# Kernel optimization log

Measured on AMD Instinct MI355X. Metric: run time of the kernel, lower is better.

Reference implementation:

```python
import jax, jax.numpy as jnp
import numpy as np

B, S, P, D, H, L, DF, O = 8, 1024, 128, 256, 4, 4, 1024, 10
DH = D // H  # 64
EPS = 1e-5


def get_positional_embeddings(seq_len, d):
    i = np.arange(seq_len, dtype=np.float64)[:, None]
    j = np.arange(d, dtype=np.float64)[None, :]
    even = np.sin(i / 10000 ** (j / d))
    odd = np.cos(i / 10000 ** ((j - 1) / d))
    return jnp.asarray(np.where(j % 2 == 0, even, odd), dtype=jnp.float32)


def layernorm(x, g, b):
    m = jnp.mean(x, axis=-1, keepdims=True)
    v = jnp.mean(jnp.square(x - m), axis=-1, keepdims=True)
    return (x - m) * jax.lax.rsqrt(v + EPS) * g + b


def setup_inputs() -> dict:
    key = jax.random.key(0)
    ks = jax.random.split(key, 20)
    w = lambda k, shp: (jax.random.normal(k, shp, dtype=jnp.float32) * 0.02)
    return {
        "images": jax.random.normal(ks[0], (B, S, P), dtype=jnp.float32),
        "Wp": w(ks[1], (D, P)), "bp": jnp.zeros((D,), jnp.float32),
        "cls": jax.random.uniform(ks[2], (1, D), dtype=jnp.float32),
        "pos": get_positional_embeddings(S + 1, D),
        "ln1_g": jnp.ones((L, D), jnp.float32), "ln1_b": jnp.zeros((L, D), jnp.float32),
        "Wq": w(ks[3], (L, H, DH, DH)), "bq": jnp.zeros((L, H, DH), jnp.float32),
        "Wk": w(ks[4], (L, H, DH, DH)), "bk": jnp.zeros((L, H, DH), jnp.float32),
        "Wv": w(ks[5], (L, H, DH, DH)), "bv": jnp.zeros((L, H, DH), jnp.float32),
        "ln2_g": jnp.ones((L, D), jnp.float32), "ln2_b": jnp.zeros((L, D), jnp.float32),
        "W1": w(ks[6], (L, DF, D)), "b1": jnp.zeros((L, DF), jnp.float32),
        "W2": w(ks[7], (L, D, DF)), "b2": jnp.zeros((L, D), jnp.float32),
        "Wo": w(ks[8], (O, D)), "bo": jnp.zeros((O,), jnp.float32),
    }


def msa(x, Wq, bq, Wk, bk, Wv, bv):
    b, s, _ = x.shape
    xh = x.reshape(b, s, H, DH)  # split heads along feature dim
    # torch Linear: y = x @ W.T + b, per head
    q = jnp.einsum("bshd,hed->bhse", xh, Wq) + bq[None, :, None, :]
    k = jnp.einsum("bshd,hed->bhse", xh, Wk) + bk[None, :, None, :]
    v = jnp.einsum("bshd,hed->bhse", xh, Wv) + bv[None, :, None, :]
    scores = jnp.einsum("bhqd,bhkd->bhqk", q, k) / (DH ** 0.5)
    attn = jax.nn.softmax(scores, axis=-1)
    out = jnp.einsum("bhqk,bhkd->bhqd", attn, v)  # [b,h,s,dh]
    return out.transpose(0, 2, 1, 3).reshape(b, s, D)  # hstack heads


def reference(images, Wp, bp, cls, pos, ln1_g, ln1_b, Wq, bq, Wk, bk, Wv, bv,
              ln2_g, ln2_b, W1, b1, W2, b2, Wo, bo):
    tokens = jnp.einsum("bsp,dp->bsd", images, Wp) + bp
    x = jnp.concatenate([jnp.broadcast_to(cls[None], (B, 1, D)), tokens], axis=1)
    x = x + pos[None]
    for l in range(L):
        x = x + msa(layernorm(x, ln1_g[l], ln1_b[l]), Wq[l], bq[l], Wk[l], bk[l], Wv[l], bv[l])
        h = layernorm(x, ln2_g[l], ln2_b[l])
        h = jax.nn.gelu(jnp.einsum("bsd,fd->bsf", h, W1[l]) + b1[l], approximate=False)
        x = x + jnp.einsum("bsf,df->bsd", h, W2[l]) + b2[l]
    logits = x[:, 0] @ Wo.T + bo
    return jax.nn.softmax(logits, axis=-1)
```

## Files before the change

kernel.cpp:

```cpp
#include <hip/hip_runtime.h>
#include <hip/hip_bf16.h>
#include <cmath>

constexpr int B  = 8;
constexpr int S  = 1024;
constexpr int P  = 128;
constexpr int D  = 256;
constexpr int H  = 4;
constexpr int L  = 4;
constexpr int DF = 1024;
constexpr int O  = 10;
constexpr int DH = D / H;
constexpr int SP = S + 1;
constexpr int N  = B * SP;
constexpr int KVPAD = 1088;

typedef short bf16x8 __attribute__((ext_vector_type(8)));
typedef float f32x4 __attribute__((ext_vector_type(4)));
typedef float f32x16 __attribute__((ext_vector_type(16)));
typedef unsigned int u32;
typedef unsigned short u16;

static __device__ __forceinline__ u16 f2b(float f) {
    __hip_bfloat16 h = __float2bfloat16(f);
    u16 u; __builtin_memcpy(&u, &h, 2);
    return u;
}
static __device__ __forceinline__ float b2f(u16 u) {
    u32 uu = (u32)u << 16; float f; __builtin_memcpy(&f, &uu, 4);
    return f;
}
static __device__ __forceinline__ u32 pk2(float a, float b) {
    return (u32)f2b(a) | ((u32)f2b(b) << 16);
}
static __device__ __forceinline__ void gload_lds16(const void* g, void* l) {
    __builtin_amdgcn_global_load_lds((const __attribute__((address_space(1))) unsigned int*)g,
                                     (__attribute__((address_space(3))) unsigned int*)l, 16, 0, 0);
}

__global__ void cvt_all(const float* __restrict__ s0, u16* __restrict__ d0, int n0,
                        const float* __restrict__ s1, u16* __restrict__ d1, int n1,
                        const float* __restrict__ s2, u16* __restrict__ d2, int n2,
                        const float* __restrict__ s3, u16* __restrict__ d3, int n3) {
    int y = blockIdx.y;
    const float* s = y == 0 ? s0 : y == 1 ? s1 : y == 2 ? s2 : s3;
    u16* d = y == 0 ? d0 : y == 1 ? d1 : y == 2 ? d2 : d3;
    int n = y == 0 ? n0 : y == 1 ? n1 : y == 2 ? n2 : n3;
    int i = blockIdx.x * 256 + threadIdx.x;
    if (i < n) {
        float4 v = ((const float4*)s)[i];
        ushort4 o;
        o.x = f2b(v.x); o.y = f2b(v.y); o.z = f2b(v.z); o.w = f2b(v.w);
        ((ushort4*)d)[i] = o;
    }
}

__global__ void build_wqkv(const float* __restrict__ Wq, const float* __restrict__ bq,
                           const float* __restrict__ Wk, const float* __restrict__ bk,
                           const float* __restrict__ Wv, const float* __restrict__ bv,
                           u16* __restrict__ Wout, float* __restrict__ bout) {
    int r = blockIdx.x, l = blockIdx.y, c = threadIdx.x;
    int sec = r >> 8;
    int ef = r & 255, h = ef >> 6, e = ef & 63;
    const float* W  = sec == 0 ? Wq : sec == 1 ? Wk : Wv;
    const float* bi = sec == 0 ? bq : sec == 1 ? bk : bv;
    float scale = sec == 0 ? 0.125f * 1.4426950408889634f : 1.0f;
    float val = ((c >> 6) == h) ? W[(((size_t)l * H + h) * 64 + e) * 64 + (c & 63)] * scale : 0.f;
    Wout[((size_t)l * 768 + r) * 256 + c] = f2b(val);
    if (c == 0) bout[(size_t)l * 768 + r] = bi[((size_t)l * H + h) * 64 + e] * scale;
}

template <int EPI>
__global__ __launch_bounds__(256) void gemm_bf16(
        const u16* __restrict__ X, const u16* __restrict__ W,
        const float* __restrict__ bias, const float* __restrict__ pos,
        float* __restrict__ Yf, u16* __restrict__ Yb,
        int M, int F, int K, int kLen) {
    __shared__ u16 Al[2][64 * 64];
    __shared__ u16 Bl[2][128 * 64];
    const int t = threadIdx.x;
    const int m0 = blockIdx.y * 64, f0 = blockIdx.x * 128;
    const int w = t >> 6, l = t & 63;
    const int wm = w >> 1, wn = w & 1;
    const int q = l & 15, g = l >> 4;
    const int kOff = blockIdx.z * kLen;
    const int lr8 = l >> 3, lp = l & 7;

    f32x4 acc[2][4];
    const f32x4 zz = {0.f, 0.f, 0.f, 0.f};
#pragma unroll
    for (int i = 0; i < 2; ++i)
#pragma unroll
        for (int j = 0; j < 4; ++j) acc[i][j] = zz;

    auto stage = [&](int sb, int kbase) {
#pragma unroll
        for (int i = 0; i < 2; ++i) {
            int ca = w + 4 * i;
            int row = ca * 8 + lr8;
            int j = lp ^ (row & 7);
            gload_lds16(X + (size_t)(m0 + row) * K + kbase + j * 8, &Al[sb][ca * 512]);
        }
#pragma unroll
        for (int i = 0; i < 4; ++i) {
            int cb = w + 4 * i;
            int row = cb * 8 + lr8;
            int j = lp ^ (row & 7);
            gload_lds16(W + (size_t)(f0 + row) * K + kbase + j * 8, &Bl[sb][cb * 512]);
        }
    };

    const int nt = kLen / 64;
    stage(0, kOff);
    __syncthreads();
    int sb = 0;
    for (int ts = 0; ts < nt; ++ts) {
        if (ts + 1 < nt) stage(sb ^ 1, kOff + (ts + 1) * 64);
#pragma unroll
        for (int kk = 0; kk < 2; ++kk) {
            bf16x8 a[2], bfr[4];
#pragma unroll
            for (int fi = 0; fi < 2; ++fi) {
                int row = wm * 32 + fi * 16 + q;
                a[fi] = *(const bf16x8*)&Al[sb][row * 64 + (((kk * 4 + g) ^ (row & 7)) * 8)];
            }
#pragma unroll
            for (int fj = 0; fj < 4; ++fj) {
                int row = wn * 64 + fj * 16 + q;
                bfr[fj] = *(const bf16x8*)&Bl[sb][row * 64 + (((kk * 4 + g) ^ (row & 7)) * 8)];
            }
#pragma unroll
            for (int fi = 0; fi < 2; ++fi)
#pragma unroll
                for (int fj = 0; fj < 4; ++fj)
                    acc[fi][fj] = __builtin_amdgcn_mfma_f32_16x16x32_bf16(a[fi], bfr[fj], acc[fi][fj], 0, 0, 0);
        }
        __syncthreads();
        sb ^= 1;
    }

#pragma unroll
    for (int fi = 0; fi < 2; ++fi) {
#pragma unroll
        for (int r = 0; r < 4; ++r) {
            int m = m0 + wm * 32 + fi * 16 + g * 4 + r;
            if (m >= M) continue;
#pragma unroll
            for (int fj = 0; fj < 4; ++fj) {
                int f = f0 + wn * 64 + fj * 16 + q;
                float val = acc[fi][fj][r];
                if constexpr (EPI == 0) {
                    val += bias[f];
                    int s = m & 1023, bb = m >> 10;
                    size_t n = (size_t)bb * SP + s + 1;
                    Yf[n * D + f] = val + pos[(size_t)(s + 1) * D + f];
                } else if constexpr (EPI == 1) {
                    val += bias[f];
                    float gel = 0.5f * val * (1.0f + erff(val * 0.70710678118654752f));
                    Yb[(size_t)m * F + f] = f2b(gel);
                } else if constexpr (EPI == 3) {
                    val += bias[f];
                    Yb[(size_t)m * F + f] = f2b(val);
                } else {
                    Yb[(size_t)blockIdx.z * M * F + (size_t)m * F + f] = f2b(val);
                }
            }
        }
    }
}

__global__ void transpose_v(const u16* __restrict__ qkv, u16* __restrict__ VTg) {
    __shared__ u16 tile[64][70];
    int bh = blockIdx.y, t0 = blockIdx.x * 64;
    int b = bh >> 2, h = bh & 3;
    int t = threadIdx.x;
    int r = t >> 3, c8 = (t & 7) * 8;
#pragma unroll
    for (int it = 0; it < 2; ++it) {
        int sp = t0 + it * 32 + r; if (sp > S) sp = S;
        uint4 v = *(const uint4*)(qkv + ((size_t)b * SP + sp) * 768 + 512 + h * 64 + c8);
        u32* dst = (u32*)&tile[it * 32 + r][c8];
        const u32* pv = (const u32*)&v;
#pragma unroll
        for (int k = 0; k < 4; ++k) dst[k] = pv[k];
    }
    __syncthreads();
#pragma unroll
    for (int it = 0; it < 2; ++it) {
        int d = it * 32 + (t >> 3);
        int spc = (t & 7) * 8;
        u16 tmp[8];
#pragma unroll
        for (int j = 0; j < 8; ++j) tmp[j] = tile[spc + j][d];
        *(uint4*)(VTg + ((size_t)bh * 64 + d) * KVPAD + t0 + spc) = *(const uint4*)tmp;
    }
}

__global__ void ln_first(const float* __restrict__ cls, const float* __restrict__ pos,
                         const float* __restrict__ gw, const float* __restrict__ bw,
                         float* __restrict__ x, u16* __restrict__ dst) {
    int row = blockIdx.x * 4 + (threadIdx.x >> 6);
    int l = threadIdx.x & 63;
    float4 v;
    if ((row % SP) == 0) {
        float4 c = *(const float4*)(cls + l * 4);
        float4 pp = *(const float4*)(pos + l * 4);
        v.x = c.x + pp.x; v.y = c.y + pp.y; v.z = c.z + pp.z; v.w = c.w + pp.w;
        *(float4*)(x + (size_t)row * D + l * 4) = v;
    } else {
        v = *(const float4*)(x + (size_t)row * D + l * 4);
    }
    float s = v.x + v.y + v.z + v.w;
    for (int off = 32; off; off >>= 1) s += __shfl_xor(s, off, 64);
    float mean = s * (1.0f / D);
    float dx0 = v.x - mean, dx1 = v.y - mean, dx2 = v.z - mean, dx3 = v.w - mean;
    float sq = dx0 * dx0 + dx1 * dx1 + dx2 * dx2 + dx3 * dx3;
    for (int off = 32; off; off >>= 1) sq += __shfl_xor(sq, off, 64);
    float rs = rsqrtf(sq * (1.0f / D) + 1e-5f);
    float4 gv = *(const float4*)(gw + l * 4);
    float4 bv = *(const float4*)(bw + l * 4);
    ushort4 o;
    o.x = f2b(dx0 * rs * gv.x + bv.x);
    o.y = f2b(dx1 * rs * gv.y + bv.y);
    o.z = f2b(dx2 * rs * gv.z + bv.z);
    o.w = f2b(dx3 * rs * gv.w + bv.w);
    *(ushort4*)(dst + (size_t)row * D + l * 4) = o;
}

__global__ __launch_bounds__(512, 4) void attn_stage(const u16* __restrict__ qkv,
                                                     const u16* __restrict__ VTg,
                                                     u16* __restrict__ opart,
                                                     float* __restrict__ lsum,
                                                     int nqt) {
    const int qg = blockIdx.x, bh = blockIdx.y, quarter = blockIdx.z;
    const int h4 = bh & 3, b = bh >> 2;
    const int t = threadIdx.x;
    const int wv = t >> 6, l = t & 63;
    const int col = l & 31, hh = l >> 5;

    __shared__ u16 Kl[5 * 64 * 64];
    __shared__ u16 Vl[5 * 64 * 64];

    const int kv_start = quarter * 256;
    const int kv_len = (quarter == 3) ? (SP - 768) : 256;
    const int ntiles = (kv_len + 63) >> 6;

    const int qt = qg * 8 + wv;
    const int q0w = qt * 32;

    bf16x8 qf[4];
    {
        int qr = q0w + col; if (qr > S) qr = S;
        const u16* qp = qkv + ((size_t)b * SP + qr) * 768 + h4 * 64 + hh * 8;
#pragma unroll
        for (int c = 0; c < 4; ++c) qf[c] = *(const bf16x8*)(qp + c * 16);
    }

    {
        const int rloc = wv * 8 + (l >> 3);
        const int j = (l & 7) ^ (((rloc >> 3) ^ rloc) & 7);
        for (int tt = 0; tt < ntiles; ++tt) {
            int krow = kv_start + tt * 64 + rloc; if (krow > S) krow = S;
            gload_lds16(qkv + ((size_t)b * SP + krow) * 768 + 256 + h4 * 64 + j * 8,
                        &Kl[(tt * 8 + wv) * 512]);
            gload_lds16(VTg + ((size_t)bh * 64 + rloc) * KVPAD + kv_start + tt * 64 + j * 8,
                        &Vl[(tt * 8 + wv) * 512]);
        }
    }
    __syncthreads();
    if (qt >= nqt) return;

    const int swA = ((col >> 3) ^ col) & 7;
    const int swB = swA ^ 4;

    f32x16 o0, o1;
#pragma unroll
    for (int r = 0; r < 16; ++r) { o0[r] = 0.f; o1[r] = 0.f; }
    float l_run = 0.f;

    for (int tile = 0; tile < ntiles; ++tile) {
        const int kv0 = tile * 64;
        const u16* Kt = &Kl[tile * 4096];
        const u16* Vt = &Vl[tile * 4096];

        f32x16 s0, s1;
#pragma unroll
        for (int r = 0; r < 16; ++r) { s0[r] = 0.f; s1[r] = 0.f; }
        __builtin_amdgcn_s_setprio(1);
#pragma unroll
        for (int c = 0; c < 4; ++c) {
            bf16x8 k0 = *(const bf16x8*)&Kt[col * 64 + (((2 * c + hh) ^ swA) * 8)];
            bf16x8 k1 = *(const bf16x8*)&Kt[(32 + col) * 64 + (((2 * c + hh) ^ swB) * 8)];
            s0 = __builtin_amdgcn_mfma_f32_32x32x16_bf16(k0, qf[c], s0, 0, 0, 0);
            s1 = __builtin_amdgcn_mfma_f32_32x32x16_bf16(k1, qf[c], s1, 0, 0, 0);
        }
        __builtin_amdgcn_s_setprio(0);

        float p[32];
#pragma unroll
        for (int r = 0; r < 16; ++r) { p[r] = s0[r]; p[16 + r] = s1[r]; }

        if (kv0 + 64 > kv_len) {
#pragma unroll
            for (int kvs = 0; kvs < 2; ++kvs)
#pragma unroll
                for (int r = 0; r < 16; ++r) {
                    int kvloc = kvs * 32 + (r & 3) + 8 * (r >> 2) + 4 * hh;
                    if (kv0 + kvloc >= kv_len) p[kvs * 16 + r] = -1e30f;
                }
        }

#pragma unroll
        for (int j = 0; j < 32; ++j) p[j] = exp2f(p[j]);
        {
            float t16[16];
#pragma unroll
            for (int j = 0; j < 16; ++j) t16[j] = p[2 * j] + p[2 * j + 1];
#pragma unroll
            for (int j = 0; j < 8; ++j) t16[j] = t16[j] + t16[j + 8];
#pragma unroll
            for (int j = 0; j < 4; ++j) t16[j] = t16[j] + t16[j + 4];
            l_run += (t16[0] + t16[1]) + (t16[2] + t16[3]);
        }

        __builtin_amdgcn_s_setprio(1);
#pragma unroll
        for (int kvs = 0; kvs < 2; ++kvs) {
            u32 pk[8];
#pragma unroll
            for (int i = 0; i < 8; ++i) pk[i] = pk2(p[kvs * 16 + 2 * i], p[kvs * 16 + 2 * i + 1]);
            u32 ex[4];
#pragma unroll
            for (int kk = 0; kk < 4; ++kk) {
                const int k = (kk < 2) ? kk : kk + 2;
                u32 send = hh ? pk[k] : pk[k + 2];
                ex[kk] = (u32)__shfl_xor((int)send, 32);
            }
#pragma unroll
            for (int cc = 0; cc < 2; ++cc) {
                union { u32 u[4]; bf16x8 v; } pa;
                u32 e0 = ex[cc * 2], e1 = ex[cc * 2 + 1];
                pa.u[0] = hh ? e0 : pk[4 * cc];
                pa.u[1] = hh ? e1 : pk[4 * cc + 1];
                pa.u[2] = hh ? pk[4 * cc + 2] : e0;
                pa.u[3] = hh ? pk[4 * cc + 3] : e1;
                int lch = kvs * 4 + cc * 2 + hh;
                bf16x8 v0 = *(const bf16x8*)&Vt[col * 64 + ((lch ^ swA) * 8)];
                bf16x8 v1 = *(const bf16x8*)&Vt[(32 + col) * 64 + ((lch ^ swB) * 8)];
                o0 = __builtin_amdgcn_mfma_f32_32x32x16_bf16(pa.v, v0, o0, 0, 0, 0);
                o1 = __builtin_amdgcn_mfma_f32_32x32x16_bf16(pa.v, v1, o1, 0, 0, 0);
            }
        }
        __builtin_amdgcn_s_setprio(0);
    }

    float l_full = l_run + __shfl_xor(l_run, 32);
    const size_t obase = ((size_t)quarter * 32 + bh) * SP;
#pragma unroll
    for (int r = 0; r < 16; ++r) {
        int qrow = (r & 3) + 8 * (r >> 2) + 4 * hh;
        int qq = q0w + qrow;
        if (qq < SP) {
            opart[(obase + qq) * 64 + col]      = f2b(o0[r]);
            opart[(obase + qq) * 64 + 32 + col] = f2b(o1[r]);
        }
    }
    if (l < 32) {
        int qq = q0w + l;
        if (qq < SP) lsum[obase + qq] = l_full;
    }
}

__global__ void combine_ln2(const u16* __restrict__ opart, const float* __restrict__ lsum,
                            const float* __restrict__ gw, const float* __restrict__ bw,
                            float* __restrict__ x, u16* __restrict__ lnb) {
    int row = blockIdx.x * 4 + (threadIdx.x >> 6);
    int l = threadIdx.x & 63;
    int b = row / SP, qq = row % SP;
    int h = l >> 4, d0 = (l * 4) & 63;
    int bh = b * 4 + h;
    float csum = 0.f, a0 = 0.f, a1 = 0.f, a2 = 0.f, a3 = 0.f;
#pragma unroll
    for (int i = 0; i < 4; ++i) {
        size_t idx = ((size_t)i * 32 + bh) * SP + qq;
        csum += lsum[idx];
        ushort4 ov = *(const ushort4*)&opart[idx * 64 + d0];
        a0 += b2f(ov.x); a1 += b2f(ov.y); a2 += b2f(ov.z); a3 += b2f(ov.w);
    }
    float inv = 1.0f / csum;
    float4 xv = *(const float4*)(x + (size_t)row * D + l * 4);
    xv.x += a0 * inv; xv.y += a1 * inv; xv.z += a2 * inv; xv.w += a3 * inv;
    *(float4*)(x + (size_t)row * D + l * 4) = xv;

    float s = xv.x + xv.y + xv.z + xv.w;
    for (int off = 32; off; off >>= 1) s += __shfl_xor(s, off, 64);
    float mean = s * (1.0f / D);
    float dx0 = xv.x - mean, dx1 = xv.y - mean, dx2 = xv.z - mean, dx3 = xv.w - mean;
    float sq = dx0 * dx0 + dx1 * dx1 + dx2 * dx2 + dx3 * dx3;
    for (int off = 32; off; off >>= 1) sq += __shfl_xor(sq, off, 64);
    float rs = rsqrtf(sq * (1.0f / D) + 1e-5f);
    float4 gv = *(const float4*)(gw + l * 4);
    float4 bv = *(const float4*)(bw + l * 4);
    ushort4 o;
    o.x = f2b(dx0 * rs * gv.x + bv.x);
    o.y = f2b(dx1 * rs * gv.y + bv.y);
    o.z = f2b(dx2 * rs * gv.z + bv.z);
    o.w = f2b(dx3 * rs * gv.w + bv.w);
    *(ushort4*)(lnb + (size_t)row * D + l * 4) = o;
}

__global__ void combine2_ln1(const u16* __restrict__ Pkb, const float* __restrict__ b2,
                             const float* __restrict__ gw, const float* __restrict__ bw,
                             float* __restrict__ x, u16* __restrict__ lnb) {
    int row = blockIdx.x * 4 + (threadIdx.x >> 6);
    int l = threadIdx.x & 63;
    ushort4 p0 = *(const ushort4*)(Pkb + (size_t)row * D + l * 4);
    ushort4 p1 = *(const ushort4*)(Pkb + (size_t)N * D + (size_t)row * D + l * 4);
    float4 bv2 = *(const float4*)(b2 + l * 4);
    float4 xv = *(const float4*)(x + (size_t)row * D + l * 4);
    xv.x += b2f(p0.x) + b2f(p1.x) + bv2.x;
    xv.y += b2f(p0.y) + b2f(p1.y) + bv2.y;
    xv.z += b2f(p0.z) + b2f(p1.z) + bv2.z;
    xv.w += b2f(p0.w) + b2f(p1.w) + bv2.w;
    *(float4*)(x + (size_t)row * D + l * 4) = xv;

    float s = xv.x + xv.y + xv.z + xv.w;
    for (int off = 32; off; off >>= 1) s += __shfl_xor(s, off, 64);
    float mean = s * (1.0f / D);
    float dx0 = xv.x - mean, dx1 = xv.y - mean, dx2 = xv.z - mean, dx3 = xv.w - mean;
    float sq = dx0 * dx0 + dx1 * dx1 + dx2 * dx2 + dx3 * dx3;
    for (int off = 32; off; off >>= 1) sq += __shfl_xor(sq, off, 64);
    float rs = rsqrtf(sq * (1.0f / D) + 1e-5f);
    float4 gv = *(const float4*)(gw + l * 4);
    float4 bv = *(const float4*)(bw + l * 4);
    ushort4 o;
    o.x = f2b(dx0 * rs * gv.x + bv.x);
    o.y = f2b(dx1 * rs * gv.y + bv.y);
    o.z = f2b(dx2 * rs * gv.z + bv.z);
    o.w = f2b(dx3 * rs * gv.w + bv.w);
    *(ushort4*)(lnb + (size_t)row * D + l * 4) = o;
}

__global__ void tail_fused(const u16* __restrict__ opart, const float* __restrict__ lsum,
                           const float* __restrict__ x,
                           const float* __restrict__ g2, const float* __restrict__ b2w,
                           const u16* __restrict__ W1l, const float* __restrict__ b1l,
                           const u16* __restrict__ W2l, const float* __restrict__ b2l,
                           const float* __restrict__ Wo, const float* __restrict__ bo,
                           float* __restrict__ out) {
    __shared__ float ln[256];
    __shared__ float hbuf[1024];
    __shared__ float xc[256];
    __shared__ float red[4];
    __shared__ float logits[O];
    const int b = blockIdx.x, t = threadIdx.x;
    const int h = t >> 6, dl = t & 63;

    float csum = 0.f, a = 0.f;
#pragma unroll
    for (int i = 0; i < 4; ++i) {
        size_t idx = ((size_t)i * 32 + b * 4 + h) * SP;
        csum += lsum[idx];
        a += b2f(opart[idx * 64 + dl]);
    }
    float xv = x[(size_t)b * SP * D + t] + a / csum;
    xc[t] = xv;

    float s = xv;
    for (int off = 32; off; off >>= 1) s += __shfl_xor(s, off, 64);
    if ((t & 63) == 0) red[t >> 6] = s;
    __syncthreads();
    float mean = (red[0] + red[1] + red[2] + red[3]) * (1.0f / D);
    float dx = xv - mean;
    float sq = dx * dx;
    for (int off = 32; off; off >>= 1) sq += __shfl_xor(sq, off, 64);
    __syncthreads();
    if ((t & 63) == 0) red[t >> 6] = sq;
    __syncthreads();
    float var = (red[0] + red[1] + red[2] + red[3]) * (1.0f / D);
    ln[t] = dx * rsqrtf(var + 1e-5f) * g2[t] + b2w[t];
    __syncthreads();

#pragma unroll
    for (int i = 0; i < 4; ++i) {
        int f = t + i * 256;
        const u16* wr = W1l + (size_t)f * D;
        float acc = b1l[f];
        for (int d = 0; d < D; d += 8) {
            bf16x8 wv = *(const bf16x8*)(wr + d);
            const u16* wu = (const u16*)&wv;
#pragma unroll
            for (int j = 0; j < 8; ++j) acc += ln[d + j] * b2f(wu[j]);
        }
        hbuf[f] = 0.5f * acc * (1.0f + erff(acc * 0.70710678118654752f));
    }
    __syncthreads();

    {
        const u16* wr = W2l + (size_t)t * DF;
        float acc = b2l[t];
        for (int f = 0; f < DF; f += 8) {
            bf16x8 wv = *(const bf16x8*)(wr + f);
            const u16* wu = (const u16*)&wv;
#pragma unroll
            for (int j = 0; j < 8; ++j) acc += hbuf[f + j] * b2f(wu[j]);
        }
        xc[t] += acc;
    }
    __syncthreads();

    if (t < O) {
        float acc = bo[t];
        const float* wr = Wo + (size_t)t * D;
        for (int d = 0; d < D; ++d) acc += xc[d] * wr[d];
        logits[t] = acc;
    }
    __syncthreads();
    if (t == 0) {
        float mx = logits[0];
        for (int o = 1; o < O; ++o) mx = fmaxf(mx, logits[o]);
        float ssum = 0.f, e[O];
        for (int o = 0; o < O; ++o) { e[o] = expf(logits[o] - mx); ssum += e[o]; }
        float inv = 1.0f / ssum;
        for (int o = 0; o < O; ++o) out[b * O + o] = e[o] * inv;
    }
}

extern "C" void kernel_launch(void* const* d_in, const int* in_sizes, int n_in,
                              void* d_out, int out_size, void* d_ws, size_t ws_size,
                              hipStream_t stream) {
    const float* images = (const float*)d_in[0];
    const float* Wp     = (const float*)d_in[1];
    const float* bp     = (const float*)d_in[2];
    const float* cls    = (const float*)d_in[3];
    const float* pos    = (const float*)d_in[4];
    const float* ln1_g  = (const float*)d_in[5];
    const float* ln1_b  = (const float*)d_in[6];
    const float* Wq     = (const float*)d_in[7];
    const float* bq     = (const float*)d_in[8];
    const float* Wk     = (const float*)d_in[9];
    const float* bk     = (const float*)d_in[10];
    const float* Wv     = (const float*)d_in[11];
    const float* bv     = (const float*)d_in[12];
    const float* ln2_g  = (const float*)d_in[13];
    const float* ln2_b  = (const float*)d_in[14];
    const float* W1     = (const float*)d_in[15];
    const float* b1     = (const float*)d_in[16];
    const float* W2     = (const float*)d_in[17];
    const float* b2     = (const float*)d_in[18];
    const float* Wo     = (const float*)d_in[19];
    const float* bo     = (const float*)d_in[20];
    float* out = (float*)d_out;

    auto align256 = [](size_t v) { return (v + 255) & ~(size_t)255; };
    char* p = (char*)d_ws;
    float* x      = (float*)p; p += align256((size_t)N * D * 4);
    u16* lnb      = (u16*)p;   p += align256((size_t)N * D * 2);
    u16* qkvbuf   = (u16*)p;   p += align256((size_t)(N + 128) * 768 * 2);
    char* midop   = p;         p += align256((size_t)N * DF * 2);
    u16* Pkb      = (u16*)p;   p += align256((size_t)2 * N * D * 2);
    float* lsum   = (float*)p; p += align256((size_t)4 * 32 * SP * 4);
    u16* VTg      = (u16*)p;   p += align256((size_t)32 * 64 * KVPAD * 2);
    u16* imgb     = (u16*)p;   p += align256((size_t)B * S * P * 2);
    u16* Wpb      = (u16*)p;   p += align256((size_t)D * P * 2);
    u16* W1b      = (u16*)p;   p += align256((size_t)L * DF * D * 2);
    u16* W2b      = (u16*)p;   p += align256((size_t)L * D * DF * 2);
    u16* Wqkvb    = (u16*)p;   p += align256((size_t)L * 768 * 256 * 2);
    float* bqkvf  = (float*)p; p += align256((size_t)L * 768 * 4);
    u16* mid      = (u16*)midop;
    u16* opart    = (u16*)midop;

    cvt_all<<<dim3(1024, 4), 256, 0, stream>>>(
        images, imgb, B * S * P / 4,
        Wp, Wpb, D * P / 4,
        W1, W1b, L * DF * D / 4,
        W2, W2b, L * D * DF / 4);
    build_wqkv<<<dim3(768, L), 256, 0, stream>>>(Wq, bq, Wk, bk, Wv, bv, Wqkvb, bqkvf);

    gemm_bf16<0><<<dim3(2, 128, 1), 256, 0, stream>>>(
        imgb, Wpb, bp, pos, x, nullptr, B * S, D, P, P);
    ln_first<<<N / 4, 256, 0, stream>>>(cls, pos, ln1_g, ln1_b, x, lnb);

    for (int l = 0; l < 3; ++l) {
        gemm_bf16<3><<<dim3(6, 129, 1), 256, 0, stream>>>(
            lnb, Wqkvb + (size_t)l * 768 * 256, bqkvf + (size_t)l * 768,
            nullptr, nullptr, qkvbuf, N, 768, D, D);
        transpose_v<<<dim3(17, 32), 256, 0, stream>>>(qkvbuf, VTg);
        attn_stage<<<dim3(5, 32, 4), 512, 0, stream>>>(qkvbuf, VTg, opart, lsum, 33);
        combine_ln2<<<N / 4, 256, 0, stream>>>(opart, lsum, ln2_g + l * D, ln2_b + l * D, x, lnb);
        gemm_bf16<1><<<dim3(8, 129, 1), 256, 0, stream>>>(
            lnb, W1b + (size_t)l * DF * D, b1 + (size_t)l * DF,
            nullptr, nullptr, mid, N, DF, D, D);
        gemm_bf16<4><<<dim3(2, 129, 2), 256, 0, stream>>>(
            mid, W2b + (size_t)l * D * DF, nullptr, nullptr, nullptr, Pkb, N, D, DF, DF / 2);
        combine2_ln1<<<N / 4, 256, 0, stream>>>(Pkb, b2 + (size_t)l * D,
                                                ln1_g + (l + 1) * D, ln1_b + (l + 1) * D, x, lnb);
    }

    {
        const int l = 3;
        gemm_bf16<3><<<dim3(6, 129, 1), 256, 0, stream>>>(
            lnb, Wqkvb + (size_t)l * 768 * 256, bqkvf + (size_t)l * 768,
            nullptr, nullptr, qkvbuf, N, 768, D, D);
        transpose_v<<<dim3(17, 32), 256, 0, stream>>>(qkvbuf, VTg);
        attn_stage<<<dim3(1, 32, 4), 512, 0, stream>>>(qkvbuf, VTg, opart, lsum, 1);
        tail_fused<<<B, 256, 0, stream>>>(opart, lsum, x,
                                          ln2_g + l * D, ln2_b + l * D,
                                          W1b + (size_t)l * DF * D, b1 + (size_t)l * DF,
                                          W2b + (size_t)l * D * DF, b2 + (size_t)l * D,
                                          Wo, bo, out);
    }
}
```

Before: 359.4 us.

## Split tail fused kernel into parallel LN, MLP1, MLP2 and head kernels

The single 8-block tail kernel, which ran the CLS-token LayerNorm, both MLP matvecs and the classifier head serially in one block per batch, is split into four kernels. The two matvecs now run on 64 blocks each, with row work divided across threads and combined by warp shuffles. This spreads the latency-bound final-layer MLP over many more CUs. The cost is three extra kernel launches and intermediate round trips through global memory.

```diff
diff --git a/kernel.cpp b/kernel.cpp
--- a/kernel.cpp
+++ b/kernel.cpp
@@ -441,21 +441,13 @@
     *(ushort4*)(lnb + (size_t)row * D + l * 4) = o;
 }
 
-__global__ void tail_fused(const u16* __restrict__ opart, const float* __restrict__ lsum,
-                           const float* __restrict__ x,
-                           const float* __restrict__ g2, const float* __restrict__ b2w,
-                           const u16* __restrict__ W1l, const float* __restrict__ b1l,
-                           const u16* __restrict__ W2l, const float* __restrict__ b2l,
-                           const float* __restrict__ Wo, const float* __restrict__ bo,
-                           float* __restrict__ out) {
-    __shared__ float ln[256];
-    __shared__ float hbuf[1024];
-    __shared__ float xc[256];
+__global__ void tail_ln(const u16* __restrict__ opart, const float* __restrict__ lsum,
+                        const float* __restrict__ x,
+                        const float* __restrict__ g2, const float* __restrict__ b2w,
+                        float* __restrict__ xc, float* __restrict__ lnc) {
     __shared__ float red[4];
-    __shared__ float logits[O];
     const int b = blockIdx.x, t = threadIdx.x;
     const int h = t >> 6, dl = t & 63;
-
     float csum = 0.f, a = 0.f;
 #pragma unroll
     for (int i = 0; i < 4; ++i) {
@@ -464,7 +456,7 @@
         a += b2f(opart[idx * 64 + dl]);
     }
     float xv = x[(size_t)b * SP * D + t] + a / csum;
-    xc[t] = xv;
+    xc[b * D + t] = xv;
 
     float s = xv;
     for (int off = 32; off; off >>= 1) s += __shfl_xor(s, off, 64);
@@ -478,51 +470,82 @@
     if ((t & 63) == 0) red[t >> 6] = sq;
     __syncthreads();
     float var = (red[0] + red[1] + red[2] + red[3]) * (1.0f / D);
-    ln[t] = dx * rsqrtf(var + 1e-5f) * g2[t] + b2w[t];
-    __syncthreads();
-
-#pragma unroll
-    for (int i = 0; i < 4; ++i) {
-        int f = t + i * 256;
-        const u16* wr = W1l + (size_t)f * D;
-        float acc = b1l[f];
-        for (int d = 0; d < D; d += 8) {
-            bf16x8 wv = *(const bf16x8*)(wr + d);
-            const u16* wu = (const u16*)&wv;
-#pragma unroll
-            for (int j = 0; j < 8; ++j) acc += ln[d + j] * b2f(wu[j]);
-        }
-        hbuf[f] = 0.5f * acc * (1.0f + erff(acc * 0.70710678118654752f));
-    }
-    __syncthreads();
-
-    {
-        const u16* wr = W2l + (size_t)t * DF;
-        float acc = b2l[t];
-        for (int f = 0; f < DF; f += 8) {
-            bf16x8 wv = *(const bf16x8*)(wr + f);
-            const u16* wu = (const u16*)&wv;
-#pragma unroll
-            for (int j = 0; j < 8; ++j) acc += hbuf[f + j] * b2f(wu[j]);
-        }
-        xc[t] += acc;
-    }
-    __syncthreads();
-
-    if (t < O) {
-        float acc = bo[t];
-        const float* wr = Wo + (size_t)t * D;
-        for (int d = 0; d < D; ++d) acc += xc[d] * wr[d];
-        logits[t] = acc;
-    }
-    __syncthreads();
-    if (t == 0) {
-        float mx = logits[0];
-        for (int o = 1; o < O; ++o) mx = fmaxf(mx, logits[o]);
-        float ssum = 0.f, e[O];
-        for (int o = 0; o < O; ++o) { e[o] = expf(logits[o] - mx); ssum += e[o]; }
-        float inv = 1.0f / ssum;
-        for (int o = 0; o < O; ++o) out[b * O + o] = e[o] * inv;
+    lnc[b * D + t] = dx * rsqrtf(var + 1e-5f) * g2[t] + b2w[t];
+}
+
+__global__ void tail_mlp1(const float* __restrict__ lnc,
+                          const u16* __restrict__ W1l, const float* __restrict__ b1l,
+                          float* __restrict__ midc) {
+    __shared__ float ln[256];
+    const int fc = blockIdx.x, b = blockIdx.y, t = threadIdx.x;
+    ln[t] = lnc[b * D + t];
+    __syncthreads();
+    const int f = fc * 128 + (t >> 1);
+    const int half = t & 1;
+    const u16* wr = W1l + (size_t)f * D + half * 128;
+    const float* lp = &ln[half * 128];
+    float acc = 0.f;
+#pragma unroll
+    for (int d = 0; d < 128; d += 8) {
+        bf16x8 wv = *(const bf16x8*)(wr + d);
+        const u16* wu = (const u16*)&wv;
+#pragma unroll
+        for (int j = 0; j < 8; ++j) acc += lp[d + j] * b2f(wu[j]);
+    }
+    acc += __shfl_xor(acc, 1);
+    if (half == 0) {
+        float v = acc + b1l[f];
+        midc[b * DF + f] = 0.5f * v * (1.0f + erff(v * 0.70710678118654752f));
+    }
+}
+
+__global__ void tail_mlp2(const float* __restrict__ midc,
+                          const u16* __restrict__ W2l, const float* __restrict__ b2l,
+                          const float* __restrict__ xc, float* __restrict__ xc2) {
+    __shared__ float mh[1024];
+    const int dc = blockIdx.x, b = blockIdx.y, t = threadIdx.x;
+#pragma unroll
+    for (int i = 0; i < 4; ++i) mh[t + i * 256] = midc[b * DF + t + i * 256];
+    __syncthreads();
+    const int dout = dc * 32 + (t >> 3);
+    const int oct = t & 7;
+    const u16* wr = W2l + (size_t)dout * DF + oct * 128;
+    const float* mp = &mh[oct * 128];
+    float acc = 0.f;
+#pragma unroll
+    for (int f = 0; f < 128; f += 8) {
+        bf16x8 wv = *(const bf16x8*)(wr + f);
+        const u16* wu = (const u16*)&wv;
+#pragma unroll
+        for (int j = 0; j < 8; ++j) acc += mp[f + j] * b2f(wu[j]);
+    }
+    acc += __shfl_xor(acc, 1);
+    acc += __shfl_xor(acc, 2);
+    acc += __shfl_xor(acc, 4);
+    if (oct == 0) xc2[b * D + dout] = xc[b * D + dout] + acc + b2l[dout];
+}
+
+__global__ void head_kernel(const float* __restrict__ xc,
+                            const float* __restrict__ Wo,
+                            const float* __restrict__ bo,
+                            float* __restrict__ out) {
+    __shared__ float logits[B][O];
+    int t = threadIdx.x;
+    if (t < B * O) {
+        int b = t / O, o = t % O;
+        const float* xr = xc + (size_t)b * D;
+        float acc = bo[o];
+        for (int d = 0; d < D; ++d) acc += xr[d] * Wo[(size_t)o * D + d];
+        logits[b][o] = acc;
+    }
+    __syncthreads();
+    if (t < B) {
+        float mx = -1e30f;
+        for (int o = 0; o < O; ++o) mx = fmaxf(mx, logits[t][o]);
+        float s = 0.f, e[O];
+        for (int o = 0; o < O; ++o) { e[o] = expf(logits[t][o] - mx); s += e[o]; }
+        float inv = 1.0f / s;
+        for (int o = 0; o < O; ++o) out[t * O + o] = e[o] * inv;
     }
 }
 
@@ -567,6 +590,10 @@
     u16* W2b      = (u16*)p;   p += align256((size_t)L * D * DF * 2);
     u16* Wqkvb    = (u16*)p;   p += align256((size_t)L * 768 * 256 * 2);
     float* bqkvf  = (float*)p; p += align256((size_t)L * 768 * 4);
+    float* xc     = (float*)p; p += align256((size_t)B * D * 4);
+    float* lnc    = (float*)p; p += align256((size_t)B * D * 4);
+    float* midc   = (float*)p; p += align256((size_t)B * DF * 4);
+    float* xc2    = (float*)p; p += align256((size_t)B * D * 4);
     u16* mid      = (u16*)midop;
     u16* opart    = (u16*)midop;
 
@@ -604,10 +631,11 @@
             nullptr, nullptr, qkvbuf, N, 768, D, D);
         transpose_v<<<dim3(17, 32), 256, 0, stream>>>(qkvbuf, VTg);
         attn_stage<<<dim3(1, 32, 4), 512, 0, stream>>>(qkvbuf, VTg, opart, lsum, 1);
-        tail_fused<<<B, 256, 0, stream>>>(opart, lsum, x,
-                                          ln2_g + l * D, ln2_b + l * D,
-                                          W1b + (size_t)l * DF * D, b1 + (size_t)l * DF,
-                                          W2b + (size_t)l * D * DF, b2 + (size_t)l * D,
-                                          Wo, bo, out);
-    }
-}
+        tail_ln<<<B, 256, 0, stream>>>(opart, lsum, x, ln2_g + l * D, ln2_b + l * D, xc, lnc);
+        tail_mlp1<<<dim3(8, B), 256, 0, stream>>>(lnc, W1b + (size_t)l * DF * D,
+                                                  b1 + (size_t)l * DF, midc);
+        tail_mlp2<<<dim3(8, B), 256, 0, stream>>>(midc, W2b + (size_t)l * D * DF,
+                                                  b2 + (size_t)l * D, xc, xc2);
+        head_kernel<<<1, 256, 0, stream>>>(xc2, Wo, bo, out);
+    }
+}
```

After: 335.0 us. -6.8%, faster.
